# Kernel tuning notes

Hardware: AMD Instinct MI355X
Metric: run time of the kernel (lower is better)

The kernel has to match this reference:

```python
import jax, jax.numpy as jnp
import numpy as np

GROUPS = 8
HEADS = 8
EPS = 1e-5


def group_norm(x, w, b, groups=GROUPS, eps=EPS):
    # x: [B, C, D, H, W]
    B, C, D, H, W = x.shape
    xg = x.reshape(B, groups, C // groups, D, H, W)
    mu = xg.mean(axis=(2, 3, 4, 5), keepdims=True)
    var = xg.var(axis=(2, 3, 4, 5), keepdims=True)
    xn = ((xg - mu) / jnp.sqrt(var + eps)).reshape(B, C, D, H, W)
    return xn * w[None, :, None, None, None] + b[None, :, None, None, None]


def conv1x1(x, w, b):
    # 1x1x1 Conv3d == channel-mixing GEMM. w: [Cout, Cin], x: [B, Cin, D, H, W]
    y = jnp.einsum('oc,bcdhw->bodhw', w, x)
    return y + b[None, :, None, None, None]


def setup_inputs() -> dict:
    key = jax.random.key(0)
    ks = jax.random.split(key, 8)
    C, CTX = 512, 512
    B, D, H, W = 1, 16, 16, 16
    x = jax.random.normal(ks[0], (B, C, D, H, W), dtype=jnp.float32)
    context = jax.random.normal(ks[1], (B, CTX, D, H, W), dtype=jnp.float32)
    return {
        'x': x,
        'context': context,
        'norm_w': jnp.ones((C,), jnp.float32),
        'norm_b': jnp.zeros((C,), jnp.float32),
        'normc_w': jnp.ones((CTX,), jnp.float32),
        'normc_b': jnp.zeros((CTX,), jnp.float32),
        'q_w': jax.random.normal(ks[2], (C, C), jnp.float32) * 0.02,
        'q_b': jnp.zeros((C,), jnp.float32),
        'kv_w': jax.random.normal(ks[3], (2 * C, CTX), jnp.float32) * 0.02,
        'kv_b': jnp.zeros((2 * C,), jnp.float32),
        'proj_w': jax.random.normal(ks[4], (C, C), jnp.float32) * 0.02,
        'proj_b': jnp.zeros((C,), jnp.float32),
    }


def _split_heads(t, heads):
    # [B, (h c), D, H, W] -> [B, h, S, c] with S = D*H*W
    B, C, D, H, W = t.shape
    return t.reshape(B, heads, C // heads, D * H * W).transpose(0, 1, 3, 2)


def reference(x, context, norm_w, norm_b, normc_w, normc_b,
              q_w, q_b, kv_w, kv_b, proj_w, proj_b):
    B, C, D, H, W = x.shape
    h = group_norm(x, norm_w, norm_b)
    c = group_norm(context, normc_w, normc_b)
    q = conv1x1(h, q_w, q_b)
    kv = conv1x1(c, kv_w, kv_b)
    k, v = jnp.split(kv, 2, axis=1)
    q = _split_heads(q, HEADS)   # [B, h, S, c]
    k = _split_heads(k, HEADS)
    v = _split_heads(v, HEADS)
    scale = (C // HEADS) ** (-0.5)
    logits = jnp.einsum('bhqc,bhkc->bhqk', q, k) * scale
    attn = jax.nn.softmax(logits, axis=-1)
    out = jnp.einsum('bhqk,bhkc->bhqc', attn, v)
    # [B, h, S, c] -> [B, (h c), D, H, W]
    out = out.transpose(0, 1, 3, 2).reshape(B, C, D, H, W)
    out = conv1x1(out, proj_w, proj_b)
    return x + out
```

## Files before the change

kernel.cpp:

```cpp
#include <hip/hip_runtime.h>

typedef unsigned short u16;
typedef unsigned int u32;
typedef float f32x4 __attribute__((ext_vector_type(4)));
typedef __bf16 bf16x8 __attribute__((ext_vector_type(8)));
typedef u32 u32x4 __attribute__((ext_vector_type(4)));
typedef u32 u32x2 __attribute__((ext_vector_type(2)));
typedef short s16x4 __attribute__((ext_vector_type(4)));

#define LOG2E 1.44269504088896340736f

static __device__ __forceinline__ u16 f2bf(float f){ u32 u=__builtin_bit_cast(u32,f); u32 r=u+0x7fffu+((u>>16)&1u); return (u16)(r>>16); }
static __device__ __forceinline__ u32 pk2(float a,float b){ return (u32)f2bf(a)|((u32)f2bf(b)<<16); }
static __device__ __forceinline__ float fexp2(float x){
#if __has_builtin(__builtin_amdgcn_exp2f)
  return __builtin_amdgcn_exp2f(x);
#else
  float r; asm volatile("v_exp_f32 %0, %1" : "=v"(r) : "v"(x)); return r;
#endif
}
static __device__ __forceinline__ f32x4 mfma16(u32x4 a,u32x4 b,f32x4 c){
  return __builtin_amdgcn_mfma_f32_16x16x32_bf16(__builtin_bit_cast(bf16x8,a),__builtin_bit_cast(bf16x8,b),c,0,0,0);
}
#if __has_builtin(__builtin_amdgcn_mfma_f32_16x16x16bf16_1k)
static __device__ __forceinline__ f32x4 mfma1k(s16x4 a,s16x4 b,f32x4 c){
  return __builtin_amdgcn_mfma_f32_16x16x16bf16_1k(a,b,c,0,0,0);
}
#else
static __device__ __forceinline__ f32x4 mfma1k(s16x4 a,s16x4 b,f32x4 c){
  f32x4 d; asm("v_mfma_f32_16x16x16_bf16 %0, %1, %2, %3":"=v"(d):"v"(a),"v"(b),"v"(c)); return d;
}
#endif
static __device__ __forceinline__ u32x4 ld16(const u32* p){ return *(const u32x4*)p; }
static __device__ __forceinline__ s16x4 ld8(const u32* p){
  return __builtin_bit_cast(s16x4, *(const u32x2*)p);
}
static __device__ __forceinline__ void stlds(u32* d, uint4 v){
  *(uint2*)d = make_uint2(v.x,v.y); *(uint2*)(d+2) = make_uint2(v.z,v.w);
}
static __device__ __forceinline__ uint4 pack8(float4 a,float4 b){
  uint4 o; o.x=pk2(a.x,a.y); o.y=pk2(a.z,a.w); o.z=pk2(b.x,b.y); o.w=pk2(b.z,b.w); return o;
}

__global__ __launch_bounds__(256) void k_stats(const float* __restrict__ x, const float* __restrict__ c,
                                               float* __restrict__ stats){
  const int g=blockIdx.x>>3;
  const float* src=(g<8?x:c)+(size_t)(g&7)*262144+(size_t)(blockIdx.x&7)*32768;
  const float4* p=(const float4*)src;
  const int t=threadIdx.x;
  float s1=0.f,s2=0.f;
  for(int i=0;i<32;i++){
    float4 v=p[t+i*256];
    s1+=v.x+v.y+v.z+v.w;
    s2+=v.x*v.x+v.y*v.y+v.z*v.z+v.w*v.w;
  }
  #pragma unroll
  for(int m=1;m<64;m<<=1){ s1+=__shfl_xor(s1,m,64); s2+=__shfl_xor(s2,m,64); }
  __shared__ float r1[4],r2[4];
  const int lane=t&63,w=t>>6;
  if(lane==0){ r1[w]=s1; r2[w]=s2; }
  __syncthreads();
  if(t==0){
    stats[blockIdx.x*2  ]=r1[0]+r1[1]+r1[2]+r1[3];
    stats[blockIdx.x*2+1]=r2[0]+r2[1]+r2[2]+r2[3];
  }
}

__global__ __launch_bounds__(256) void k_norm(const float* __restrict__ x,const float* __restrict__ ctx,
    const float* __restrict__ qw,const float* __restrict__ kvw,const float* __restrict__ pw,
    const float* __restrict__ nw,const float* __restrict__ nb,
    const float* __restrict__ ncw,const float* __restrict__ ncb,
    const float* __restrict__ stats,
    u16* __restrict__ xnT,u16* __restrict__ cnT,u16* __restrict__ Wall){
  const int bid=blockIdx.x, t=threadIdx.x;
  if(bid>=256){
    const int wb=bid-256;
    const float* src = wb<8 ? pw+(size_t)wb*32768 : (wb<16 ? qw+(size_t)(wb-8)*32768 : kvw+(size_t)(wb-16)*32768);
    u16* dst = Wall + (size_t)wb*32768;
    #pragma unroll
    for(int it=0;it<16;it++){
      int off = it*2048 + t*8;
      float4 a=*(const float4*)(src+off), b=*(const float4*)(src+off+4);
      *(uint4*)(dst+off) = pack8(a,b);
    }
    return;
  }
  const int op=bid>>7, r=bid&127;
  const int c0=(r>>4)*64, s0=(r&15)*256;
  const float* src = op? ctx : x;
  u16* dst = op? cnT : xnT;
  const float* anw = op? ncw : nw;
  const float* anb = op? ncb : nb;
  __shared__ float al[64], bt[64];
  __shared__ u32 T[256*37];
  if(t<64){
    int c=c0+t, g=(op?8:0)+(c>>6);
    float s1=0.f,s2=0.f;
    #pragma unroll
    for(int s=0;s<8;s++){ s1+=stats[(g*8+s)*2]; s2+=stats[(g*8+s)*2+1]; }
    float mean=s1*(1.f/262144.f);
    float var =s2*(1.f/262144.f)-mean*mean;
    float a=anw[c]*rsqrtf(var+1e-5f);
    al[t]=a; bt[t]=anb[c]-mean*a;
  }
  __syncthreads();
  const int pr=t>>3, sj=(t&7)*8;
  const float a0=al[2*pr], b0=bt[2*pr], a1=al[2*pr+1], b1=bt[2*pr+1];
  #pragma unroll
  for(int it=0;it<4;it++){
    int ls=it*64+sj;
    const float* p0=src+(size_t)(c0+2*pr)*4096+s0+ls;
    const float* p1=src+(size_t)(c0+2*pr+1)*4096+s0+ls;
    float4 va=*(const float4*)p0, vb=*(const float4*)(p0+4);
    float4 vc=*(const float4*)p1, vd=*(const float4*)(p1+4);
    float f0[8]={va.x,va.y,va.z,va.w,vb.x,vb.y,vb.z,vb.w};
    float f1[8]={vc.x,vc.y,vc.z,vc.w,vd.x,vd.y,vd.z,vd.w};
    #pragma unroll
    for(int j=0;j<8;j++)
      T[(ls+j)*37+pr]=pk2(a0*f0[j]+b0, a1*f1[j]+b1);
  }
  __syncthreads();
  #pragma unroll
  for(int ps=0;ps<8;ps++){
    int row = ps*32 + (t>>3);
    const u32* rp=&T[row*37+(t&7)*4];
    u32 v0=rp[0],v1=rp[1],v2=rp[2],v3=rp[3];
    *(uint4*)(dst + (size_t)(s0+row)*512 + c0 + (t&7)*8) = make_uint4(v0,v1,v2,v3);
  }
}

template<int EPI,int BG,int ZS>
__global__ __launch_bounds__(256,2) void k_gemm(const u16* __restrict__ A0,const u16* __restrict__ A1,
    const u16* __restrict__ B0,const u16* __restrict__ B1,
    const float* __restrict__ bias0,const float* __restrict__ bias1,
    const float* __restrict__ residf,void* __restrict__ out0,void* __restrict__ out1,
    float scale0,float scale1){
  __shared__ __align__(16) u32 As[2][128*20];
  __shared__ __align__(16) u32 Bs[2][128*20];
  const int t=threadIdx.x, lane=t&63, w=t>>6;
  const int wm=w&1, wn=w>>1, quad=lane>>4, l15=lane&15;
  const int bid=blockIdx.x;
  const int z = ZS ? (bid>>7) : 0;
  const int r = ZS ? (bid&127) : bid;
  const u16* A = z? A1:A0;
  const u16* B = z? B1:B0;
  const float* bias = z? bias1:bias0;
  void* outv = z? out1:out0;
  const float scale = z? scale1:scale0;
  int m0,n0;
  if(EPI==0){ m0=(r>>2)*128; n0=(r&3)*128; }
  else      { m0=(r>>5)*128; n0=(r&31)*128; }
  const int arow=t>>1, ak=(t&1)*16;
  uint4 a0,a1,b0,b1;
  auto loadAB=[&](int kk){
    const u16* ap=A+(size_t)(m0+arow)*512+kk+ak;
    a0=*(const uint4*)ap; a1=*(const uint4*)(ap+8);
    const u16* bp;
    if(BG) bp = B + ((size_t)((kk>>6)*4096 + n0+arow))*64 + (kk&63) + ak;
    else   bp = B + (size_t)(n0+arow)*512 + kk + ak;
    b0=*(const uint4*)bp; b1=*(const uint4*)(bp+8);
  };
  auto writeAB=[&](int bsel){
    u32* aw=&As[bsel][arow*20+(ak>>1)];
    stlds(aw,a0); stlds(aw+4,a1);
    u32* bw=&Bs[bsel][arow*20+(ak>>1)];
    stlds(bw,b0); stlds(bw+4,b1);
  };
  f32x4 acc[4][4];
  #pragma unroll
  for(int i=0;i<4;i++)
    #pragma unroll
    for(int j=0;j<4;j++){ acc[i][j].x=0.f; acc[i][j].y=0.f; acc[i][j].z=0.f; acc[i][j].w=0.f; }
  auto compute=[&](int bsel){
    const u32* Ab=&As[bsel][(wm*64+l15)*20+quad*4];
    const u32* Bb=&Bs[bsel][(wn*64+l15)*20+quad*4];
    u32x4 af[4], bf[4];
    #pragma unroll
    for(int mt=0;mt<4;mt++) af[mt]=ld16(Ab+mt*320);
    #pragma unroll
    for(int nt=0;nt<4;nt++) bf[nt]=ld16(Bb+nt*320);
    #pragma unroll
    for(int mt=0;mt<4;mt++)
      #pragma unroll
      for(int nt=0;nt<4;nt++) acc[mt][nt]=mfma16(af[mt],bf[nt],acc[mt][nt]);
  };
  loadAB(0); writeAB(0);
  __syncthreads();
  for(int kk=0;kk<512;kk+=64){
    loadAB(kk+32);
    compute(0);
    writeAB(1);
    __syncthreads();
    const bool n2=(kk+64)<512;
    if(n2) loadAB(kk+64);
    compute(1);
    if(n2){ writeAB(0); __syncthreads(); }
  }
  #pragma unroll
  for(int mt=0;mt<4;mt++)
    #pragma unroll
    for(int nt=0;nt<4;nt++){
      const int n = n0 + wn*64 + nt*16 + l15;
      if(EPI==0){
        u16* out=(u16*)outv;
        const float bn=bias[n];
        const size_t base=((size_t)((n>>6)*4096))*64+(size_t)(n&63);
        #pragma unroll
        for(int r4=0;r4<4;r4++){
          int m=m0+wm*64+mt*16+quad*4+r4;
          out[base+(size_t)m*64]=f2bf((acc[mt][nt][r4]+bn)*scale);
        }
      }else if(EPI==1){
        u16* out=(u16*)outv;
        #pragma unroll
        for(int r4=0;r4<4;r4++){
          int m=m0+wm*64+mt*16+quad*4+r4;
          out[(size_t)m*4096+n]=f2bf(acc[mt][nt][r4]+bias[m]);
        }
      }else{
        float* out=(float*)outv;
        #pragma unroll
        for(int r4=0;r4<4;r4++){
          int m=m0+wm*64+mt*16+quad*4+r4;
          out[(size_t)m*4096+n]=acc[mt][nt][r4]+bias[m]+residf[(size_t)m*4096+n];
        }
      }
    }
}

__global__ __launch_bounds__(512) void k_attn(const u16* __restrict__ Qh,const u16* __restrict__ Kh,
                                              const u16* __restrict__ Vp,u16* __restrict__ Oh){
  __shared__ __align__(16) u32 KS[2][2][64*36];
  __shared__ __align__(16) u32 VS[2][2][64*36];
  const int t=threadIdx.x, lane=t&63, w=t>>6, quad=lane>>4, l15=lane&15;
  const int half=w>>2, wq=w&3;
  const int h=blockIdx.y, q0=blockIdx.x*128;
  const int tt=t&255, srow=tt>>2, sc=(tt&3)*16;
  const u16* Kg = Kh + ((size_t)(h*4096 + half*2048 + srow))*64 + sc;
  const u16* Vg = Vp + (size_t)(h*64+srow)*4096 + half*2048 + sc;
  u32x4 qf[2][2];
  #pragma unroll
  for(int qt=0;qt<2;qt++){
    const u32* Qg=(const u32*)(Qh + ((size_t)(h*4096+q0+qt*64+wq*16+l15))*64);
    qf[qt][0]=ld16(Qg+quad*4);
    qf[qt][1]=ld16(Qg+16+quad*4);
  }
  uint4 pk0,pk1,pv0,pv1;
  auto loadKV=[&](int t0l){
    const u16* kp=Kg+(size_t)t0l*64;
    pk0=*(const uint4*)kp; pk1=*(const uint4*)(kp+8);
    const u16* vp=Vg+t0l;
    pv0=*(const uint4*)vp; pv1=*(const uint4*)(vp+8);
  };
  auto writeKV=[&](u32* Kb,u32* Vb){
    u32* kw=Kb+srow*36+(sc>>1);
    stlds(kw,pk0); stlds(kw+4,pk1);
    u32* vw=Vb+srow*36+(sc>>1);
    stlds(vw,pv0); stlds(vw+4,pv1);
  };
  float lrun[2]={0.f,0.f};
  f32x4 oacc[2][4];
  #pragma unroll
  for(int qt=0;qt<2;qt++)
    #pragma unroll
    for(int cn=0;cn<4;cn++){ oacc[qt][cn].x=0.f; oacc[qt][cn].y=0.f; oacc[qt][cn].z=0.f; oacc[qt][cn].w=0.f; }

  auto tilestep=[&](const u32* Kb,const u32* Vb){
    f32x4 sv[2][4];
    #pragma unroll
    for(int nt=0;nt<4;nt++){
      const u32* kb=Kb+(nt*16+l15)*36+quad*4;
      u32x4 k0=ld16(kb), k1=ld16(kb+16);
      #pragma unroll
      for(int qt=0;qt<2;qt++){
        f32x4 a; a.x=0.f; a.y=0.f; a.z=0.f; a.w=0.f;
        a=mfma16(k0,qf[qt][0],a);
        sv[qt][nt]=mfma16(k1,qf[qt][1],a);
      }
    }
    s16x4 pfr[2][4];
    #pragma unroll
    for(int qt=0;qt<2;qt++)
      #pragma unroll
      for(int nt=0;nt<4;nt++){
        float p0=fexp2(sv[qt][nt].x),p1=fexp2(sv[qt][nt].y),p2=fexp2(sv[qt][nt].z),p3=fexp2(sv[qt][nt].w);
        lrun[qt]+=(p0+p1)+(p2+p3);
        u32x2 pp;
        pp.x=(__builtin_bit_cast(u32,p0)>>16)|(__builtin_bit_cast(u32,p1)&0xffff0000u);
        pp.y=(__builtin_bit_cast(u32,p2)>>16)|(__builtin_bit_cast(u32,p3)&0xffff0000u);
        pfr[qt][nt]=__builtin_bit_cast(s16x4,pp);
      }
    #pragma unroll
    for(int cn=0;cn<4;cn++){
      const u32* vb=Vb+(cn*16+l15)*36+quad*2;
      f32x4 a0=oacc[0][cn], a1=oacc[1][cn];
      #pragma unroll
      for(int nt=0;nt<4;nt++){
        s16x4 vf=ld8(vb+nt*8);
        a0=mfma1k(pfr[0][nt],vf,a0);
        a1=mfma1k(pfr[1][nt],vf,a1);
      }
      oacc[0][cn]=a0; oacc[1][cn]=a1;
    }
  };

  loadKV(0); writeKV(KS[half][0],VS[half][0]);
  __syncthreads();
  for(int t0=0;t0<2048;t0+=128){
    loadKV(t0+64);
    tilestep(KS[half][0],VS[half][0]);
    writeKV(KS[half][1],VS[half][1]);
    __syncthreads();
    const bool more=(t0+128)<2048;
    if(more) loadKV(t0+128);
    tilestep(KS[half][1],VS[half][1]);
    if(more){ writeKV(KS[half][0],VS[half][0]); __syncthreads(); }
  }
  __syncthreads();
  float* cb=(float*)KS;
  const int cbi=(wq*64+lane)*34;
  if(half==1){
    #pragma unroll
    for(int qt=0;qt<2;qt++)
      #pragma unroll
      for(int cn=0;cn<4;cn++)
        #pragma unroll
        for(int r4=0;r4<4;r4++) cb[cbi+qt*16+cn*4+r4]=oacc[qt][cn][r4];
    cb[cbi+32]=lrun[0]; cb[cbi+33]=lrun[1];
  }
  __syncthreads();
  if(half==0){
    #pragma unroll
    for(int qt=0;qt<2;qt++){
      #pragma unroll
      for(int cn=0;cn<4;cn++)
        #pragma unroll
        for(int r4=0;r4<4;r4++) oacc[qt][cn][r4]+=cb[cbi+qt*16+cn*4+r4];
      float l=lrun[qt]+cb[cbi+32+qt];
      l+=__shfl_xor(l,16,64);
      l+=__shfl_xor(l,32,64);
      #pragma unroll
      for(int r4=0;r4<4;r4++){
        float inv=1.f/__shfl(l,quad*4+r4,64);
        #pragma unroll
        for(int cn=0;cn<4;cn++)
          Oh[((size_t)(h*4096+q0+qt*64+wq*16+quad*4+r4))*64 + cn*16 + l15]=f2bf(oacc[qt][cn][r4]*inv);
      }
    }
  }
}

extern "C" void kernel_launch(void* const* d_in, const int* in_sizes, int n_in,
                              void* d_out, int out_size, void* d_ws, size_t ws_size,
                              hipStream_t stream){
  (void)in_sizes; (void)n_in; (void)out_size; (void)ws_size;
  const float* x  =(const float*)d_in[0];
  const float* ctx=(const float*)d_in[1];
  const float* nw =(const float*)d_in[2];
  const float* nb =(const float*)d_in[3];
  const float* ncw=(const float*)d_in[4];
  const float* ncb=(const float*)d_in[5];
  const float* qw =(const float*)d_in[6];
  const float* qb =(const float*)d_in[7];
  const float* kvw=(const float*)d_in[8];
  const float* kvb=(const float*)d_in[9];
  const float* pw =(const float*)d_in[10];
  const float* pb =(const float*)d_in[11];
  float* out=(float*)d_out;
  char* ws=(char*)d_ws;
  float* stats=(float*)ws;
  u16* Wall=(u16*)(ws+1024);
  u16* pwb  = Wall;
  u16* qwb  = Wall+262144;
  u16* kvw1b= Wall+524288;
  u16* kvw2b= Wall+786432;
  u16* cnT=(u16*)(ws+2098176);
  u16* xnT=(u16*)(ws+6292480);
  u16* Qh =(u16*)(ws+10486784);
  u16* Kh =(u16*)(ws+14681088);
  u16* Vp =(u16*)(ws+6292480);
  u16* Oh =(u16*)(ws+2098176);

  k_stats<<<dim3(128),dim3(256),0,stream>>>(x,ctx,stats);
  k_norm<<<dim3(288),dim3(256),0,stream>>>(x,ctx,qw,kvw,pw,nw,nb,ncw,ncb,stats,xnT,cnT,Wall);
  k_gemm<0,0,1><<<dim3(256),dim3(256),0,stream>>>(xnT,cnT,qwb,kvw1b,qb,kvb,nullptr,Qh,Kh,0.125f*LOG2E,1.f);
  k_gemm<1,0,0><<<dim3(128),dim3(256),0,stream>>>(kvw2b,nullptr,cnT,nullptr,kvb+512,nullptr,nullptr,Vp,nullptr,1.f,1.f);
  k_attn<<<dim3(32,8),dim3(512),0,stream>>>(Qh,Kh,Vp,Oh);
  k_gemm<2,1,0><<<dim3(128),dim3(256),0,stream>>>(pwb,nullptr,Oh,nullptr,pb,nullptr,x,out,nullptr,1.f,1.f);
}
```

Before: 187.6 us.

## Halve GEMM M-tile to 64 rows, double grid, and retune LDS padding

The GEMM kernel's M tile shrinks from 128 to 64 rows, so each warp computes 2x4 MFMA tiles instead of 4x4 and every GEMM launch uses twice as many blocks. The aim is more parallelism across CUs for these small GEMMs. The load mapping is reworked so each thread fetches one 16-byte A chunk and two B chunks, and the LDS row stride drops from 20 to 18 words, with fragments read as two 8-byte loads. The attention kernel's K/V LDS stride likewise changes from 36 to 34 words, using the same split fragment loads to alter bank mapping. The cost is less data reuse per block and more total global traffic for the B operand.

```diff
diff --git a/kernel.cpp b/kernel.cpp
--- a/kernel.cpp
+++ b/kernel.cpp
@@ -31,6 +31,10 @@
   f32x4 d; asm("v_mfma_f32_16x16x16_bf16 %0, %1, %2, %3":"=v"(d):"v"(a),"v"(b),"v"(c)); return d;
 }
 #endif
+static __device__ __forceinline__ u32x4 ldfrag(const u32* p){
+  uint2 a=*(const uint2*)p; uint2 b=*(const uint2*)(p+2);
+  u32x4 r; r.x=a.x; r.y=a.y; r.z=b.x; r.w=b.y; return r;
+}
 static __device__ __forceinline__ u32x4 ld16(const u32* p){ return *(const u32x4*)p; }
 static __device__ __forceinline__ s16x4 ld8(const u32* p){
   return __builtin_bit_cast(s16x4, *(const u32x2*)p);
@@ -130,57 +134,60 @@
 }
 
 template<int EPI,int BG,int ZS>
-__global__ __launch_bounds__(256,2) void k_gemm(const u16* __restrict__ A0,const u16* __restrict__ A1,
+__global__ __launch_bounds__(256) void k_gemm(const u16* __restrict__ A0,const u16* __restrict__ A1,
     const u16* __restrict__ B0,const u16* __restrict__ B1,
     const float* __restrict__ bias0,const float* __restrict__ bias1,
     const float* __restrict__ residf,void* __restrict__ out0,void* __restrict__ out1,
     float scale0,float scale1){
-  __shared__ __align__(16) u32 As[2][128*20];
-  __shared__ __align__(16) u32 Bs[2][128*20];
+  __shared__ __align__(16) u32 As[2][64*18];
+  __shared__ __align__(16) u32 Bs[2][128*18];
   const int t=threadIdx.x, lane=t&63, w=t>>6;
   const int wm=w&1, wn=w>>1, quad=lane>>4, l15=lane&15;
   const int bid=blockIdx.x;
-  const int z = ZS ? (bid>>7) : 0;
-  const int r = ZS ? (bid&127) : bid;
+  const int z = ZS ? (bid>>8) : 0;
+  const int r = ZS ? (bid&255) : bid;
   const u16* A = z? A1:A0;
   const u16* B = z? B1:B0;
   const float* bias = z? bias1:bias0;
   void* outv = z? out1:out0;
   const float scale = z? scale1:scale0;
   int m0,n0;
-  if(EPI==0){ m0=(r>>2)*128; n0=(r&3)*128; }
-  else      { m0=(r>>5)*128; n0=(r&31)*128; }
-  const int arow=t>>1, ak=(t&1)*16;
-  uint4 a0,a1,b0,b1;
+  if(EPI==0){ m0=(r>>2)*64; n0=(r&3)*128; }
+  else      { m0=(r>>5)*64; n0=(r&31)*128; }
+  const int arow=t>>2, ak=(t&3)*8;
+  uint4 a0,b0,b1;
   auto loadAB=[&](int kk){
-    const u16* ap=A+(size_t)(m0+arow)*512+kk+ak;
-    a0=*(const uint4*)ap; a1=*(const uint4*)(ap+8);
-    const u16* bp;
-    if(BG) bp = B + ((size_t)((kk>>6)*4096 + n0+arow))*64 + (kk&63) + ak;
-    else   bp = B + (size_t)(n0+arow)*512 + kk + ak;
-    b0=*(const uint4*)bp; b1=*(const uint4*)(bp+8);
+    a0=*(const uint4*)(A+(size_t)(m0+arow)*512+kk+ak);
+    const u16 *bp0,*bp1;
+    if(BG){
+      bp0 = B + ((size_t)((kk>>6)*4096 + n0+arow))*64 + (kk&63) + ak;
+      bp1 = B + ((size_t)((kk>>6)*4096 + n0+64+arow))*64 + (kk&63) + ak;
+    }else{
+      bp0 = B + (size_t)(n0+arow)*512 + kk + ak;
+      bp1 = B + (size_t)(n0+64+arow)*512 + kk + ak;
+    }
+    b0=*(const uint4*)bp0; b1=*(const uint4*)bp1;
   };
   auto writeAB=[&](int bsel){
-    u32* aw=&As[bsel][arow*20+(ak>>1)];
-    stlds(aw,a0); stlds(aw+4,a1);
-    u32* bw=&Bs[bsel][arow*20+(ak>>1)];
-    stlds(bw,b0); stlds(bw+4,b1);
-  };
-  f32x4 acc[4][4];
-  #pragma unroll
-  for(int i=0;i<4;i++)
+    stlds(&As[bsel][arow*18+(ak>>1)],a0);
+    stlds(&Bs[bsel][arow*18+(ak>>1)],b0);
+    stlds(&Bs[bsel][(64+arow)*18+(ak>>1)],b1);
+  };
+  f32x4 acc[2][4];
+  #pragma unroll
+  for(int i=0;i<2;i++)
     #pragma unroll
     for(int j=0;j<4;j++){ acc[i][j].x=0.f; acc[i][j].y=0.f; acc[i][j].z=0.f; acc[i][j].w=0.f; }
   auto compute=[&](int bsel){
-    const u32* Ab=&As[bsel][(wm*64+l15)*20+quad*4];
-    const u32* Bb=&Bs[bsel][(wn*64+l15)*20+quad*4];
-    u32x4 af[4], bf[4];
-    #pragma unroll
-    for(int mt=0;mt<4;mt++) af[mt]=ld16(Ab+mt*320);
-    #pragma unroll
-    for(int nt=0;nt<4;nt++) bf[nt]=ld16(Bb+nt*320);
-    #pragma unroll
-    for(int mt=0;mt<4;mt++)
+    const u32* Ab=&As[bsel][(wm*32+l15)*18+quad*4];
+    const u32* Bb=&Bs[bsel][(wn*64+l15)*18+quad*4];
+    u32x4 af[2], bf[4];
+    #pragma unroll
+    for(int mt=0;mt<2;mt++) af[mt]=ldfrag(Ab+mt*288);
+    #pragma unroll
+    for(int nt=0;nt<4;nt++) bf[nt]=ldfrag(Bb+nt*288);
+    #pragma unroll
+    for(int mt=0;mt<2;mt++)
       #pragma unroll
       for(int nt=0;nt<4;nt++) acc[mt][nt]=mfma16(af[mt],bf[nt],acc[mt][nt]);
   };
@@ -197,7 +204,7 @@
     if(n2){ writeAB(0); __syncthreads(); }
   }
   #pragma unroll
-  for(int mt=0;mt<4;mt++)
+  for(int mt=0;mt<2;mt++)
     #pragma unroll
     for(int nt=0;nt<4;nt++){
       const int n = n0 + wn*64 + nt*16 + l15;
@@ -207,21 +214,21 @@
         const size_t base=((size_t)((n>>6)*4096))*64+(size_t)(n&63);
         #pragma unroll
         for(int r4=0;r4<4;r4++){
-          int m=m0+wm*64+mt*16+quad*4+r4;
+          int m=m0+wm*32+mt*16+quad*4+r4;
           out[base+(size_t)m*64]=f2bf((acc[mt][nt][r4]+bn)*scale);
         }
       }else if(EPI==1){
         u16* out=(u16*)outv;
         #pragma unroll
         for(int r4=0;r4<4;r4++){
-          int m=m0+wm*64+mt*16+quad*4+r4;
+          int m=m0+wm*32+mt*16+quad*4+r4;
           out[(size_t)m*4096+n]=f2bf(acc[mt][nt][r4]+bias[m]);
         }
       }else{
         float* out=(float*)outv;
         #pragma unroll
         for(int r4=0;r4<4;r4++){
-          int m=m0+wm*64+mt*16+quad*4+r4;
+          int m=m0+wm*32+mt*16+quad*4+r4;
           out[(size_t)m*4096+n]=acc[mt][nt][r4]+bias[m]+residf[(size_t)m*4096+n];
         }
       }
@@ -230,8 +237,8 @@
 
 __global__ __launch_bounds__(512) void k_attn(const u16* __restrict__ Qh,const u16* __restrict__ Kh,
                                               const u16* __restrict__ Vp,u16* __restrict__ Oh){
-  __shared__ __align__(16) u32 KS[2][2][64*36];
-  __shared__ __align__(16) u32 VS[2][2][64*36];
+  __shared__ __align__(16) u32 KS[2][2][64*34];
+  __shared__ __align__(16) u32 VS[2][2][64*34];
   const int t=threadIdx.x, lane=t&63, w=t>>6, quad=lane>>4, l15=lane&15;
   const int half=w>>2, wq=w&3;
   const int h=blockIdx.y, q0=blockIdx.x*128;
@@ -253,9 +260,9 @@
     pv0=*(const uint4*)vp; pv1=*(const uint4*)(vp+8);
   };
   auto writeKV=[&](u32* Kb,u32* Vb){
-    u32* kw=Kb+srow*36+(sc>>1);
+    u32* kw=Kb+srow*34+(sc>>1);
     stlds(kw,pk0); stlds(kw+4,pk1);
-    u32* vw=Vb+srow*36+(sc>>1);
+    u32* vw=Vb+srow*34+(sc>>1);
     stlds(vw,pv0); stlds(vw+4,pv1);
   };
   float lrun[2]={0.f,0.f};
@@ -269,8 +276,8 @@
     f32x4 sv[2][4];
     #pragma unroll
     for(int nt=0;nt<4;nt++){
-      const u32* kb=Kb+(nt*16+l15)*36+quad*4;
-      u32x4 k0=ld16(kb), k1=ld16(kb+16);
+      const u32* kb=Kb+(nt*16+l15)*34+quad*4;
+      u32x4 k0=ldfrag(kb), k1=ldfrag(kb+16);
       #pragma unroll
       for(int qt=0;qt<2;qt++){
         f32x4 a; a.x=0.f; a.y=0.f; a.z=0.f; a.w=0.f;
@@ -292,7 +299,7 @@
       }
     #pragma unroll
     for(int cn=0;cn<4;cn++){
-      const u32* vb=Vb+(cn*16+l15)*36+quad*2;
+      const u32* vb=Vb+(cn*16+l15)*34+quad*2;
       f32x4 a0=oacc[0][cn], a1=oacc[1][cn];
       #pragma unroll
       for(int nt=0;nt<4;nt++){
@@ -383,8 +390,8 @@
 
   k_stats<<<dim3(128),dim3(256),0,stream>>>(x,ctx,stats);
   k_norm<<<dim3(288),dim3(256),0,stream>>>(x,ctx,qw,kvw,pw,nw,nb,ncw,ncb,stats,xnT,cnT,Wall);
-  k_gemm<0,0,1><<<dim3(256),dim3(256),0,stream>>>(xnT,cnT,qwb,kvw1b,qb,kvb,nullptr,Qh,Kh,0.125f*LOG2E,1.f);
-  k_gemm<1,0,0><<<dim3(128),dim3(256),0,stream>>>(kvw2b,nullptr,cnT,nullptr,kvb+512,nullptr,nullptr,Vp,nullptr,1.f,1.f);
+  k_gemm<0,0,1><<<dim3(512),dim3(256),0,stream>>>(xnT,cnT,qwb,kvw1b,qb,kvb,nullptr,Qh,Kh,0.125f*LOG2E,1.f);
+  k_gemm<1,0,0><<<dim3(256),dim3(256),0,stream>>>(kvw2b,nullptr,cnT,nullptr,kvb+512,nullptr,nullptr,Vp,nullptr,1.f,1.f);
   k_attn<<<dim3(32,8),dim3(512),0,stream>>>(Qh,Kh,Vp,Oh);
-  k_gemm<2,1,0><<<dim3(128),dim3(256),0,stream>>>(pwb,nullptr,Oh,nullptr,pb,nullptr,x,out,nullptr,1.f,1.f);
-}
+  k_gemm<2,1,0><<<dim3(256),dim3(256),0,stream>>>(pwb,nullptr,Oh,nullptr,pb,nullptr,x,out,nullptr,1.f,1.f);
+}
```

Result: faster. 181.2 us (-3.4%).
